# Performance work log

Measured on AMD Instinct MI355X. Metric: run time of the kernel, lower is better.

The kernel has to match this reference:

```python
import jax, jax.numpy as jnp
import numpy as np
import math

B, S, D, H, L, DFF, NHEADS_OUT = 2, 1024, 1024, 16, 4, 4096, 3
DK = D // H
LN_EPS = 1e-5


def setup_inputs() -> dict:
    key = jax.random.key(0)
    ks = jax.random.split(key, 16)
    w = lambda k, shp: jax.random.normal(k, shp, dtype=jnp.float32) * 0.02
    return {
        "src": jax.random.normal(ks[0], (B, S, 1), dtype=jnp.float32),
        "emb_w": w(ks[1], (1, D)), "emb_b": jnp.zeros((D,), jnp.float32),
        "pe": w(ks[2], (S, D)),
        "Wq": w(ks[3], (L, D, D)), "bq": jnp.zeros((L, D), jnp.float32),
        "Wk": w(ks[4], (L, D, D)), "bk": jnp.zeros((L, D), jnp.float32),
        "Wv": w(ks[5], (L, D, D)), "bv": jnp.zeros((L, D), jnp.float32),
        "Wo": w(ks[6], (L, D, D)), "bo": jnp.zeros((L, D), jnp.float32),
        "fc1_w": w(ks[7], (L, D, DFF)), "fc1_b": jnp.zeros((L, DFF), jnp.float32),
        "fc2_w": w(ks[8], (L, DFF, D)), "fc2_b": jnp.zeros((L, D), jnp.float32),
        "ln1_g": jnp.ones((L, D), jnp.float32), "ln1_b": jnp.zeros((L, D), jnp.float32),
        "ln2_g": jnp.ones((L, D), jnp.float32), "ln2_b": jnp.zeros((L, D), jnp.float32),
        "hw1": w(ks[9], (NHEADS_OUT, D, D)), "hb1": jnp.zeros((NHEADS_OUT, D), jnp.float32),
        "hw2": w(ks[10], (NHEADS_OUT, D, 1)), "hb2": jnp.zeros((NHEADS_OUT, 1), jnp.float32),
    }


def _layernorm(x, g, b):
    mu = jnp.mean(x, axis=-1, keepdims=True)
    var = jnp.mean((x - mu) ** 2, axis=-1, keepdims=True)
    return (x - mu) * jax.lax.rsqrt(var + LN_EPS) * g + b


def _custom_softmax(x):
    # faithful to module's custom_softmax: max (inf->0), exp, sum + 1e-9
    m = jnp.max(x, axis=-1, keepdims=True)
    m = jnp.where(jnp.isinf(m), 0.0, m)
    e = jnp.exp(x - m)
    return e / (jnp.sum(e, axis=-1, keepdims=True) + 1e-9)


def _attention(x, Wq, bq, Wk, bk, Wv, bv, Wo, bo, mask):
    b, s, d = x.shape
    split = lambda t: t.reshape(b, s, H, DK).transpose(0, 2, 1, 3)  # [B,H,S,DK]
    q = split(x @ Wq + bq)
    k = split(x @ Wk + bk)
    v = split(x @ Wv + bv)
    scores = jnp.einsum('bhqd,bhkd->bhqk', q, k) / math.sqrt(DK)
    scores = jnp.where(mask, scores, -jnp.inf)
    probs = _custom_softmax(scores)
    out = jnp.einsum('bhqk,bhkd->bhqd', probs, v)
    out = out.transpose(0, 2, 1, 3).reshape(b, s, d)
    return out @ Wo + bo


def reference(src, emb_w, emb_b, pe, Wq, bq, Wk, bk, Wv, bv, Wo, bo,
              fc1_w, fc1_b, fc2_w, fc2_b, ln1_g, ln1_b, ln2_g, ln2_b,
              hw1, hb1, hw2, hb2):
    s = src.shape[1]
    mask = jnp.tril(jnp.ones((s, s), dtype=bool))[None, None]  # causal [1,1,S,S]
    x = src @ emb_w + emb_b          # [B,S,D]
    x = x + pe[:s]                   # learned positional encoding
    for l in range(L):
        attn = _attention(x, Wq[l], bq[l], Wk[l], bk[l], Wv[l], bv[l], Wo[l], bo[l], mask)
        h = _layernorm(x + attn, ln1_g[l], ln1_b[l])
        x = h + attn                 # quirk in original forward_step
        ff = jax.nn.relu(jax.nn.relu(x @ fc1_w[l] + fc1_b[l]) @ fc2_w[l] + fc2_b[l])
        h2 = _layernorm(x + ff, ln2_g[l], ln2_b[l])
        x = h2 + ff                  # quirk in original forward_step
    # output_size independent 2-layer heads, each -> scalar; stack on last dim
    hid = jax.nn.relu(jnp.einsum('bsd,odf->bsof', x, hw1) + hb1[None, None])  # [B,S,3,D]
    out = jnp.einsum('bsof,ofe->bsoe', hid, hw2) + hb2[None, None]            # [B,S,3,1]
    return out[..., 0]               # [B,S,3]
```

## Files before the change

### kernel.cpp

```cpp
#include <hip/hip_runtime.h>
#include <hip/hip_bf16.h>


#define BB 2
#define SS 1024
#define DD 1024
#define HH 16
#define LL 4
#define DFFC 4096
#define DKC 64

typedef __attribute__((ext_vector_type(8))) short short8;
typedef __attribute__((ext_vector_type(4))) float f32x4;

#define GLD16(gptr, ldsptr) \
    __builtin_amdgcn_global_load_lds( \
        (const __attribute__((address_space(1))) unsigned int*)(gptr), \
        (__attribute__((address_space(3))) unsigned int*)(ldsptr), 16, 0, 0)

__device__ __forceinline__ float ldin(const void* p, long long i, int isbf) {
    if (isbf) {
        unsigned int u = ((unsigned int)((const unsigned short*)p)[i]) << 16;
        return __uint_as_float(u);
    }
    return ((const float*)p)[i];
}
__device__ __forceinline__ unsigned short f2bf(float f) {
    unsigned int u = __float_as_uint(f);
    return (unsigned short)((u + 0x7FFFu + ((u >> 16) & 1u)) >> 16);
}
__device__ __forceinline__ float bf2f(unsigned short h) {
    return __uint_as_float(((unsigned int)h) << 16);
}

__global__ void k_detect(const void* __restrict__ ln1g, int* __restrict__ flag) {
    unsigned int w = *(const unsigned int*)ln1g;
    *flag = (w == 0x3F800000u) ? 0 : 1;
}

__global__ void k_embed(const void* __restrict__ src, const void* __restrict__ emb_w,
                        const void* __restrict__ emb_b, const void* __restrict__ pe,
                        float* __restrict__ x, unsigned short* __restrict__ xb,
                        const int* __restrict__ flag) {
    int row = blockIdx.x;
    int s = row & (SS - 1);
    int isbf = *flag;
    float sv = ldin(src, row, isbf);
    for (int d = threadIdx.x; d < DD; d += 256) {
        float v = sv * ldin(emb_w, d, isbf) + ldin(emb_b, d, isbf) + ldin(pe, (long long)s * DD + d, isbf);
        x[(long long)row * DD + d] = v;
        xb[(long long)row * DD + d] = f2bf(v);
    }
}

struct TSlot { const void* src; long long off; int ldw; int nrows; int ncols; long long dstoff; };
struct TArgs { TSlot s[4]; };

__global__ __launch_bounds__(256) void k_wtrans(TArgs ta, unsigned short* __restrict__ dst,
                                                const int* __restrict__ flag) {
    TSlot sl = ta.s[blockIdx.z];
    if (!sl.src) return;
    int k0 = blockIdx.x * 64, n0 = blockIdx.y * 64;
    if (k0 >= sl.nrows || n0 >= sl.ncols) return;
    int isbf = *flag;
    __shared__ float tile[64][65];
    int tid = threadIdx.x;
    int c = tid & 63, rg = tid >> 6;
    #pragma unroll
    for (int i = 0; i < 16; i++) {
        int kr = rg * 16 + i;
        tile[kr][c] = ldin(sl.src, sl.off + (long long)(k0 + kr) * sl.ldw + n0 + c, isbf);
    }
    __syncthreads();
    int nr = tid >> 2, kc = (tid & 3) * 16;
    unsigned short* dp = dst + sl.dstoff + (long long)(n0 + nr) * sl.nrows + k0 + kc;
    unsigned short h[16];
    #pragma unroll
    for (int j = 0; j < 16; j++) h[j] = f2bf(tile[kc + j][nr]);
    uint4 u0, u1;
    u0.x = h[0] | (h[1] << 16);  u0.y = h[2] | (h[3] << 16);
    u0.z = h[4] | (h[5] << 16);  u0.w = h[6] | (h[7] << 16);
    u1.x = h[8] | (h[9] << 16);  u1.y = h[10] | (h[11] << 16);
    u1.z = h[12] | (h[13] << 16); u1.w = h[14] | (h[15] << 16);
    *(uint4*)&dp[0] = u0;
    *(uint4*)&dp[8] = u1;
}

template <int NF>
__global__ __launch_bounds__(256) void k_gemm_mfma(
    const unsigned short* __restrict__ A, int lda,
    const unsigned short* __restrict__ Wt,
    const void* b0, const void* b1, const void* b2,
    long long o0, long long o1, long long o2,
    float* __restrict__ C, int ldc,
    unsigned short* __restrict__ Cb, int ldcb,
    int K, int act, int accum, const int* __restrict__ flag)
{
    const int BN = 32 * NF;
    __shared__ __align__(16) unsigned short As[2][128 * 32];
    __shared__ __align__(16) unsigned short Bs[2][BN * 32];
    int bflag = *flag;
    int tid = threadIdx.x;
    int wave = tid >> 6, lane = tid & 63, quad = lane >> 4, l16 = lane & 15;
    int wm = (wave & 1) * 64, wn = (wave >> 1) * 16 * NF;
    int bm = blockIdx.y * 128, bn = blockIdx.x * BN;
    int srow = lane >> 2;
    int scol = (lane & 3) * 8;

    f32x4 acc[4][NF];
    #pragma unroll
    for (int i = 0; i < 4; i++)
        #pragma unroll
        for (int j = 0; j < NF; j++) acc[i][j] = (f32x4){0.f, 0.f, 0.f, 0.f};

    const unsigned short* Abase = A + (size_t)bm * lda;

    auto stage = [&](int k0, int p) {
        #pragma unroll
        for (int i = 0; i < 2; i++) {
            int s = wave * 2 + i;
            GLD16(Abase + (size_t)(s * 16 + srow) * lda + k0 + scol, &As[p][(s * 16) * 32]);
        }
        if (NF == 4) {
            #pragma unroll
            for (int i = 0; i < 2; i++) {
                int s = wave * 2 + i;
                GLD16(Wt + (size_t)(bn + s * 16 + srow) * K + k0 + scol, &Bs[p][(s * 16) * 32]);
            }
        } else {
            GLD16(Wt + (size_t)(bn + wave * 16 + srow) * K + k0 + scol, &Bs[p][(wave * 16) * 32]);
        }
    };

    int nk = K >> 5;
    stage(0, 0);
    for (int it = 0; it < nk; it++) {
        int p = it & 1;
        __syncthreads();
        if (it + 1 < nk) stage((it + 1) << 5, p ^ 1);

        short8 af[4], bf[NF];
        #pragma unroll
        for (int mi = 0; mi < 4; mi++)
            af[mi] = *(const short8*)&As[p][(wm + mi * 16 + l16) * 32 + quad * 8];
        #pragma unroll
        for (int ni = 0; ni < NF; ni++)
            bf[ni] = *(const short8*)&Bs[p][(wn + ni * 16 + l16) * 32 + quad * 8];
        #pragma unroll
        for (int mi = 0; mi < 4; mi++)
            #pragma unroll
            for (int ni = 0; ni < NF; ni++)
                acc[mi][ni] = __builtin_amdgcn_mfma_f32_16x16x32_bf16(af[mi], bf[ni], acc[mi][ni], 0, 0, 0);
    }

    #pragma unroll
    for (int ni = 0; ni < NF; ni++) {
        int cn = bn + wn + ni * 16 + l16;
        float bval = 0.0f;
        if (b0) {
            int sel = cn >> 10;
            const void* bp = (sel == 0) ? b0 : (sel == 1) ? b1 : b2;
            long long oo = (sel == 0) ? o0 : (sel == 1) ? o1 : o2;
            bval = ldin(bp, oo + (cn - (sel << 10)), bflag);
        }
        #pragma unroll
        for (int mi = 0; mi < 4; mi++) {
            #pragma unroll
            for (int rr = 0; rr < 4; rr++) {
                int cm = bm + wm + mi * 16 + quad * 4 + rr;
                float v = acc[mi][ni][rr] + bval;
                if (accum) v += C[(size_t)cm * ldc + cn];
                if (act) v = fmaxf(v, 0.0f);
                if (C) C[(size_t)cm * ldc + cn] = v;
                if (Cb) Cb[(size_t)cm * ldcb + cn] = f2bf(v);
            }
        }
    }
}

__global__ __launch_bounds__(256) void k_attn(unsigned short* __restrict__ qkv)
{
    __shared__ __align__(16) unsigned short Vt[2][64 * 72];
    __shared__ __align__(16) unsigned short Ps[4][16 * 72];

    int tid = threadIdx.x;
    int wave = tid >> 6, lane = tid & 63, quad = lane >> 4, l16 = lane & 15;
    int qt = 15 - blockIdx.x;
    int bh = blockIdx.y;
    int b = bh >> 4, h = bh & 15;
    int q0 = qt * 64;
    int qbase = q0 + wave * 16;

    const unsigned short* qrow = qkv + (size_t)(b * SS + qbase + l16) * 3072 + h * DKC;
    short8 aq0 = *(const short8*)(qrow + quad * 8);
    short8 aq1 = *(const short8*)(qrow + 32 + quad * 8);

    f32x4 oacc[4];
    #pragma unroll
    for (int nt = 0; nt < 4; nt++) oacc[nt] = (f32x4){0.f, 0.f, 0.f, 0.f};
    float rsum[4] = {0.f, 0.f, 0.f, 0.f};

    int kp = tid & 31;
    int vc = (tid >> 5) * 8;
    unsigned short* pw = &Ps[wave][0];

    auto stageV = [&](int k0, int p) {
        const unsigned short* v0 = qkv + (size_t)(b * SS + k0 + 2 * kp) * 3072 + 2048 + h * DKC + vc;
        short8 s0 = *(const short8*)v0;
        short8 s1 = *(const short8*)(v0 + 3072);
        unsigned int* vt32 = (unsigned int*)&Vt[p][0];
        #pragma unroll
        for (int i = 0; i < 8; i++) {
            unsigned int pr = ((unsigned int)(unsigned short)s0[i]) |
                              (((unsigned int)(unsigned short)s1[i]) << 16);
            vt32[(vc + i) * 36 + kp] = pr;
        }
    };

    stageV(0, 0);
    for (int kt = 0; kt <= qt; kt++) {
        int k0 = kt * 64;
        int p = kt & 1;
        __syncthreads();
        if (kt < qt) stageV(k0 + 64, p ^ 1);

        short8 bk0[4], bk1[4];
        #pragma unroll
        for (int nt = 0; nt < 4; nt++) {
            const unsigned short* krow =
                qkv + (size_t)(b * SS + k0 + nt * 16 + l16) * 3072 + 1024 + h * DKC + quad * 8;
            bk0[nt] = *(const short8*)(krow);
            bk1[nt] = *(const short8*)(krow + 32);
        }

        f32x4 sacc[4];
        #pragma unroll
        for (int nt = 0; nt < 4; nt++) {
            sacc[nt] = (f32x4){0.f, 0.f, 0.f, 0.f};
            sacc[nt] = __builtin_amdgcn_mfma_f32_16x16x32_bf16(aq0, bk0[nt], sacc[nt], 0, 0, 0);
            sacc[nt] = __builtin_amdgcn_mfma_f32_16x16x32_bf16(aq1, bk1[nt], sacc[nt], 0, 0, 0);
        }

        #pragma unroll
        for (int nt = 0; nt < 4; nt++) {
            int key = k0 + nt * 16 + l16;
            #pragma unroll
            for (int rr = 0; rr < 4; rr++) {
                float pv = __expf(sacc[nt][rr] * 0.125f);
                if (key > qbase + quad * 4 + rr) pv = 0.0f;
                rsum[rr] += pv;
                pw[(quad * 4 + rr) * 72 + nt * 16 + l16] = f2bf(pv);
            }
        }

        short8 ap0 = *(const short8*)&pw[l16 * 72 + quad * 8];
        short8 ap1 = *(const short8*)&pw[l16 * 72 + 32 + quad * 8];
        #pragma unroll
        for (int nt = 0; nt < 4; nt++) {
            short8 bv0 = *(const short8*)&Vt[p][(nt * 16 + l16) * 72 + quad * 8];
            short8 bv1 = *(const short8*)&Vt[p][(nt * 16 + l16) * 72 + 32 + quad * 8];
            oacc[nt] = __builtin_amdgcn_mfma_f32_16x16x32_bf16(ap0, bv0, oacc[nt], 0, 0, 0);
            oacc[nt] = __builtin_amdgcn_mfma_f32_16x16x32_bf16(ap1, bv1, oacc[nt], 0, 0, 0);
        }
    }

    #pragma unroll
    for (int m = 1; m < 16; m <<= 1) {
        #pragma unroll
        for (int rr = 0; rr < 4; rr++)
            rsum[rr] += __shfl_xor(rsum[rr], m, 64);
    }
    float inv[4];
    #pragma unroll
    for (int rr = 0; rr < 4; rr++) inv[rr] = 1.0f / (rsum[rr] + 1e-9f);
    #pragma unroll
    for (int rr = 0; rr < 4; rr++) {
        size_t obase = (size_t)(b * SS + qbase + quad * 4 + rr) * 3072 + h * DKC;
        #pragma unroll
        for (int nt = 0; nt < 4; nt++)
            qkv[obase + nt * 16 + l16] = f2bf(oacc[nt][rr] * inv[rr]);
    }
}

__global__ __launch_bounds__(256) void k_addlnadd(float* __restrict__ x, const float* __restrict__ t,
                                                  const void* __restrict__ g, long long goff,
                                                  const void* __restrict__ bta, long long boff,
                                                  unsigned short* __restrict__ xb,
                                                  const int* __restrict__ flag)
{
    int row = blockIdx.x;
    int tid = threadIdx.x;
    int isbf = *flag;
    __shared__ float red[256];
    long long base = (long long)row * DD;

    float yv[4], tv[4];
    float lsum = 0.0f;
    #pragma unroll
    for (int i = 0; i < 4; i++) {
        int d = tid + i * 256;
        tv[i] = t[base + d];
        yv[i] = x[base + d] + tv[i];
        lsum += yv[i];
    }
    red[tid] = lsum;
    __syncthreads();
    for (int s = 128; s > 0; s >>= 1) {
        if (tid < s) red[tid] += red[tid + s];
        __syncthreads();
    }
    float mu = red[0] * (1.0f / DD);
    __syncthreads();

    float lv = 0.0f;
    #pragma unroll
    for (int i = 0; i < 4; i++) {
        float dl = yv[i] - mu;
        lv += dl * dl;
    }
    red[tid] = lv;
    __syncthreads();
    for (int s = 128; s > 0; s >>= 1) {
        if (tid < s) red[tid] += red[tid + s];
        __syncthreads();
    }
    float rs = rsqrtf(red[0] * (1.0f / DD) + 1e-5f);

    #pragma unroll
    for (int i = 0; i < 4; i++) {
        int d = tid + i * 256;
        float nrm = (yv[i] - mu) * rs * ldin(g, goff + d, isbf) + ldin(bta, boff + d, isbf);
        float xo = nrm + tv[i];
        x[base + d] = xo;
        xb[base + d] = f2bf(xo);
    }
}

__global__ __launch_bounds__(256) void k_head(const unsigned short* __restrict__ hid,
                                              const void* __restrict__ hw2,
                                              const void* __restrict__ hb2,
                                              void* __restrict__ out,
                                              const int* __restrict__ flag)
{
    int row = blockIdx.x;
    int o = blockIdx.y;
    int tid = threadIdx.x;
    int isbf = *flag;
    __shared__ float red[256];
    long long base = (long long)row * 3072 + o * 1024;
    float acc = 0.0f;
    for (int f = tid; f < DD; f += 256)
        acc += bf2f(hid[base + f]) * ldin(hw2, (long long)o * DD + f, isbf);
    red[tid] = acc;
    __syncthreads();
    for (int s = 128; s > 0; s >>= 1) {
        if (tid < s) red[tid] += red[tid + s];
        __syncthreads();
    }
    if (tid == 0) {
        float r = red[0] + ldin(hb2, o, isbf);
        long long idx = (long long)row * 3 + o;
        if (isbf) ((__hip_bfloat16*)out)[idx] = __float2bfloat16(r);
        else      ((float*)out)[idx] = r;
    }
}

extern "C" void kernel_launch(void* const* d_in, const int* in_sizes, int n_in,
                              void* d_out, int out_size, void* d_ws, size_t ws_size,
                              hipStream_t stream) {
    char* w = (char*)d_ws;
    int* flag = (int*)w;
    const size_t NA = (size_t)BB * SS * DD;
    float* x  = (float*)(w + 256);
    float* tb = x + NA;
    unsigned short* qkv = (unsigned short*)(tb + NA);
    unsigned short* hb  = qkv + (size_t)BB * SS * 3072;
    unsigned short* wbuf = hb + (size_t)BB * SS * 2048;
    unsigned short* xb = wbuf + 4 * (size_t)DD * DD;

    const long long MM = (long long)DD * DD;
    dim3 blk(256);
    TSlot z = {nullptr, 0, 1, 0, 0, 0};

    k_detect<<<1, 1, 0, stream>>>(d_in[16], flag);
    k_embed<<<BB * SS, blk, 0, stream>>>(d_in[0], d_in[1], d_in[2], d_in[3], x, xb, flag);

    for (int l = 0; l < LL; l++) {
        long long wo = (long long)l * MM;
        long long bo = (long long)l * DD;
        {
            TArgs ta = {{ {d_in[4],  wo, DD, DD, DD, 0},
                          {d_in[6],  wo, DD, DD, DD, MM},
                          {d_in[8],  wo, DD, DD, DD, 2 * MM},
                          {d_in[10], wo, DD, DD, DD, 3 * MM} }};
            k_wtrans<<<dim3(16, 16, 4), blk, 0, stream>>>(ta, wbuf, flag);
        }
        k_gemm_mfma<4><<<dim3(24, 16), blk, 0, stream>>>(
            xb, DD, wbuf, d_in[5], d_in[7], d_in[9], bo, bo, bo,
            nullptr, 0, qkv, 3072, DD, 0, 0, flag);
        k_attn<<<dim3(16, BB * HH), blk, 0, stream>>>(qkv);
        k_gemm_mfma<2><<<dim3(16, 16), blk, 0, stream>>>(
            qkv, 3072, wbuf + 3 * MM, d_in[11], d_in[11], d_in[11], bo, bo, bo,
            tb, DD, nullptr, 0, DD, 0, 0, flag);
        k_addlnadd<<<BB * SS, blk, 0, stream>>>(x, tb, d_in[16], bo, d_in[17], bo, xb, flag);
        for (int c = 0; c < 2; c++) {
            long long w1off = (long long)l * DD * DFFC + (long long)c * 2048;
            long long b1off = (long long)l * DFFC + (long long)c * 2048;
            long long w2off = (long long)l * DFFC * DD + (long long)c * 2048 * DD;
            {
                TArgs ta = {{ {d_in[12], w1off, DFFC, DD, 2048, 0},
                              {d_in[14], w2off, DD, 2048, DD, 2 * MM}, z, z }};
                k_wtrans<<<dim3(32, 32, 2), blk, 0, stream>>>(ta, wbuf, flag);
            }
            k_gemm_mfma<4><<<dim3(16, 16), blk, 0, stream>>>(
                xb, DD, wbuf, d_in[13], d_in[13], d_in[13], b1off, b1off + 1024, 0,
                nullptr, 0, hb, 2048, DD, 1, 0, flag);
            k_gemm_mfma<2><<<dim3(16, 16), blk, 0, stream>>>(
                hb, 2048, wbuf + 2 * MM,
                (c == 1) ? d_in[15] : nullptr, d_in[15], d_in[15], bo, bo, bo,
                tb, DD, nullptr, 0, 2048, (c == 1) ? 1 : 0, c, flag);
        }
        k_addlnadd<<<BB * SS, blk, 0, stream>>>(x, tb, d_in[18], bo, d_in[19], bo, xb, flag);
    }

    {
        TArgs ta = {{ {d_in[20], 0 * MM, DD, DD, DD, 0},
                      {d_in[20], 1 * MM, DD, DD, DD, MM},
                      {d_in[20], 2 * MM, DD, DD, DD, 2 * MM}, z }};
        k_wtrans<<<dim3(16, 16, 3), blk, 0, stream>>>(ta, wbuf, flag);
    }
    k_gemm_mfma<4><<<dim3(24, 16), blk, 0, stream>>>(
        xb, DD, wbuf, d_in[21], d_in[21], d_in[21], 0, 1024, 2048,
        nullptr, 0, qkv, 3072, DD, 1, 0, flag);
    k_head<<<dim3(BB * SS, 3), blk, 0, stream>>>(qkv, d_in[22], d_in[23], d_out, flag);
}
```

Measured before the change: 1.363 ms.

## Split causal attention over key range and shrink GEMM tiles for more blocks

Attention now runs as two blocks per query tile, each covering half the causal key range. Each writes unnormalized fp32 partial outputs and row sums to scratch buffers, and a new combine kernel adds the halves, normalizes, and writes bf16 into the qkv buffer. The GEMM kernel gains an M-fragment template parameter so all GEMMs use smaller 128x64 or 64x64 tiles, which doubles the grid sizes. The aim is better occupancy of the many compute units, in exchange for an extra kernel launch, fp32 partial traffic through memory, and less operand reuse per tile.

```diff
diff --git a/kernel.cpp b/kernel.cpp
--- a/kernel.cpp
+++ b/kernel.cpp
@@ -86,7 +86,7 @@
     *(uint4*)&dp[8] = u1;
 }
 
-template <int NF>
+template <int MF, int NF>
 __global__ __launch_bounds__(256) void k_gemm_mfma(
     const unsigned short* __restrict__ A, int lda,
     const unsigned short* __restrict__ Wt,
@@ -96,20 +96,21 @@
     unsigned short* __restrict__ Cb, int ldcb,
     int K, int act, int accum, const int* __restrict__ flag)
 {
+    const int BM = 32 * MF;
     const int BN = 32 * NF;
-    __shared__ __align__(16) unsigned short As[2][128 * 32];
+    __shared__ __align__(16) unsigned short As[2][BM * 32];
     __shared__ __align__(16) unsigned short Bs[2][BN * 32];
     int bflag = *flag;
     int tid = threadIdx.x;
     int wave = tid >> 6, lane = tid & 63, quad = lane >> 4, l16 = lane & 15;
-    int wm = (wave & 1) * 64, wn = (wave >> 1) * 16 * NF;
-    int bm = blockIdx.y * 128, bn = blockIdx.x * BN;
+    int wm = (wave & 1) * 16 * MF, wn = (wave >> 1) * 16 * NF;
+    int bm = blockIdx.y * BM, bn = blockIdx.x * BN;
     int srow = lane >> 2;
     int scol = (lane & 3) * 8;
 
-    f32x4 acc[4][NF];
-    #pragma unroll
-    for (int i = 0; i < 4; i++)
+    f32x4 acc[MF][NF];
+    #pragma unroll
+    for (int i = 0; i < MF; i++)
         #pragma unroll
         for (int j = 0; j < NF; j++) acc[i][j] = (f32x4){0.f, 0.f, 0.f, 0.f};
 
@@ -117,18 +118,14 @@
 
     auto stage = [&](int k0, int p) {
         #pragma unroll
-        for (int i = 0; i < 2; i++) {
-            int s = wave * 2 + i;
+        for (int i = 0; i < MF / 2; i++) {
+            int s = wave * (MF / 2) + i;
             GLD16(Abase + (size_t)(s * 16 + srow) * lda + k0 + scol, &As[p][(s * 16) * 32]);
         }
-        if (NF == 4) {
-            #pragma unroll
-            for (int i = 0; i < 2; i++) {
-                int s = wave * 2 + i;
-                GLD16(Wt + (size_t)(bn + s * 16 + srow) * K + k0 + scol, &Bs[p][(s * 16) * 32]);
-            }
-        } else {
-            GLD16(Wt + (size_t)(bn + wave * 16 + srow) * K + k0 + scol, &Bs[p][(wave * 16) * 32]);
+        #pragma unroll
+        for (int i = 0; i < NF / 2; i++) {
+            int s = wave * (NF / 2) + i;
+            GLD16(Wt + (size_t)(bn + s * 16 + srow) * K + k0 + scol, &Bs[p][(s * 16) * 32]);
         }
     };
 
@@ -139,15 +136,15 @@
         __syncthreads();
         if (it + 1 < nk) stage((it + 1) << 5, p ^ 1);
 
-        short8 af[4], bf[NF];
-        #pragma unroll
-        for (int mi = 0; mi < 4; mi++)
+        short8 af[MF], bf[NF];
+        #pragma unroll
+        for (int mi = 0; mi < MF; mi++)
             af[mi] = *(const short8*)&As[p][(wm + mi * 16 + l16) * 32 + quad * 8];
         #pragma unroll
         for (int ni = 0; ni < NF; ni++)
             bf[ni] = *(const short8*)&Bs[p][(wn + ni * 16 + l16) * 32 + quad * 8];
         #pragma unroll
-        for (int mi = 0; mi < 4; mi++)
+        for (int mi = 0; mi < MF; mi++)
             #pragma unroll
             for (int ni = 0; ni < NF; ni++)
                 acc[mi][ni] = __builtin_amdgcn_mfma_f32_16x16x32_bf16(af[mi], bf[ni], acc[mi][ni], 0, 0, 0);
@@ -164,7 +161,7 @@
             bval = ldin(bp, oo + (cn - (sel << 10)), bflag);
         }
         #pragma unroll
-        for (int mi = 0; mi < 4; mi++) {
+        for (int mi = 0; mi < MF; mi++) {
             #pragma unroll
             for (int rr = 0; rr < 4; rr++) {
                 int cm = bm + wm + mi * 16 + quad * 4 + rr;
@@ -178,7 +175,10 @@
     }
 }
 
-__global__ __launch_bounds__(256) void k_attn(unsigned short* __restrict__ qkv)
+__global__ __launch_bounds__(256) void k_attn(const unsigned short* __restrict__ qkv,
+                                              float* __restrict__ part0,
+                                              float* __restrict__ part1,
+                                              float* __restrict__ rs)
 {
     __shared__ __align__(16) unsigned short Vt[2][64 * 72];
     __shared__ __align__(16) unsigned short Ps[4][16 * 72];
@@ -187,9 +187,15 @@
     int wave = tid >> 6, lane = tid & 63, quad = lane >> 4, l16 = lane & 15;
     int qt = 15 - blockIdx.x;
     int bh = blockIdx.y;
+    int split = blockIdx.z;
     int b = bh >> 4, h = bh & 15;
     int q0 = qt * 64;
     int qbase = q0 + wave * 16;
+
+    int nk = qt + 1;
+    int half = (nk + 1) >> 1;
+    int kt0 = split ? half : 0;
+    int kt1 = split ? nk : half;
 
     const unsigned short* qrow = qkv + (size_t)(b * SS + qbase + l16) * 3072 + h * DKC;
     short8 aq0 = *(const short8*)(qrow + quad * 8);
@@ -217,12 +223,12 @@
         }
     };
 
-    stageV(0, 0);
-    for (int kt = 0; kt <= qt; kt++) {
+    if (kt0 < kt1) stageV(kt0 * 64, 0);
+    for (int kt = kt0; kt < kt1; kt++) {
         int k0 = kt * 64;
-        int p = kt & 1;
+        int p = (kt - kt0) & 1;
         __syncthreads();
-        if (kt < qt) stageV(k0 + 64, p ^ 1);
+        if (kt + 1 < kt1) stageV(k0 + 64, p ^ 1);
 
         short8 bk0[4], bk1[4];
         #pragma unroll
@@ -270,16 +276,40 @@
         for (int rr = 0; rr < 4; rr++)
             rsum[rr] += __shfl_xor(rsum[rr], m, 64);
     }
-    float inv[4];
-    #pragma unroll
-    for (int rr = 0; rr < 4; rr++) inv[rr] = 1.0f / (rsum[rr] + 1e-9f);
+    float* part = split ? part1 : part0;
     #pragma unroll
     for (int rr = 0; rr < 4; rr++) {
-        size_t obase = (size_t)(b * SS + qbase + quad * 4 + rr) * 3072 + h * DKC;
+        int q = qbase + quad * 4 + rr;
+        size_t obase = (size_t)(b * SS + q) * 1024 + h * DKC;
         #pragma unroll
         for (int nt = 0; nt < 4; nt++)
-            qkv[obase + nt * 16 + l16] = f2bf(oacc[nt][rr] * inv[rr]);
-    }
+            part[obase + nt * 16 + l16] = oacc[nt][rr];
+        if (l16 == 0)
+            rs[(((size_t)split * 2 + b) * 16 + h) * 1024 + q] = rsum[rr];
+    }
+}
+
+__global__ __launch_bounds__(256) void k_comb(const float* __restrict__ p0,
+                                              const float* __restrict__ p1,
+                                              const float* __restrict__ rs,
+                                              unsigned short* __restrict__ qkv)
+{
+    int row = blockIdx.x;
+    int b = row >> 10, q = row & 1023;
+    int tid = threadIdx.x;
+    int col = tid * 4;
+    int h = col >> 6;
+    float r0 = rs[(((size_t)0 + b) * 16 + h) * 1024 + q];
+    float r1 = rs[(((size_t)2 + b) * 16 + h) * 1024 + q];
+    float inv = 1.0f / (r0 + r1 + 1e-9f);
+    size_t base = (size_t)row * 1024 + col;
+    float4 a = *(const float4*)(p0 + base);
+    float4 c = *(const float4*)(p1 + base);
+    unsigned short* dst = qkv + (size_t)row * 3072 + col;
+    uint2 w;
+    w.x = f2bf((a.x + c.x) * inv) | (f2bf((a.y + c.y) * inv) << 16);
+    w.y = f2bf((a.z + c.z) * inv) | (f2bf((a.w + c.w) * inv) << 16);
+    *(uint2*)dst = w;
 }
 
 __global__ __launch_bounds__(256) void k_addlnadd(float* __restrict__ x, const float* __restrict__ t,
@@ -377,6 +407,7 @@
     unsigned short* hb  = qkv + (size_t)BB * SS * 3072;
     unsigned short* wbuf = hb + (size_t)BB * SS * 2048;
     unsigned short* xb = wbuf + 4 * (size_t)DD * DD;
+    float* rsbuf = (float*)(xb + NA);
 
     const long long MM = (long long)DD * DD;
     dim3 blk(256);
@@ -395,11 +426,12 @@
                           {d_in[10], wo, DD, DD, DD, 3 * MM} }};
             k_wtrans<<<dim3(16, 16, 4), blk, 0, stream>>>(ta, wbuf, flag);
         }
-        k_gemm_mfma<4><<<dim3(24, 16), blk, 0, stream>>>(
+        k_gemm_mfma<4, 2><<<dim3(48, 16), blk, 0, stream>>>(
             xb, DD, wbuf, d_in[5], d_in[7], d_in[9], bo, bo, bo,
             nullptr, 0, qkv, 3072, DD, 0, 0, flag);
-        k_attn<<<dim3(16, BB * HH), blk, 0, stream>>>(qkv);
-        k_gemm_mfma<2><<<dim3(16, 16), blk, 0, stream>>>(
+        k_attn<<<dim3(16, BB * HH, 2), blk, 0, stream>>>(qkv, tb, (float*)hb, rsbuf);
+        k_comb<<<BB * SS, blk, 0, stream>>>(tb, (float*)hb, rsbuf, qkv);
+        k_gemm_mfma<2, 2><<<dim3(16, 32), blk, 0, stream>>>(
             qkv, 3072, wbuf + 3 * MM, d_in[11], d_in[11], d_in[11], bo, bo, bo,
             tb, DD, nullptr, 0, DD, 0, 0, flag);
         k_addlnadd<<<BB * SS, blk, 0, stream>>>(x, tb, d_in[16], bo, d_in[17], bo, xb, flag);
@@ -412,10 +444,10 @@
                               {d_in[14], w2off, DD, 2048, DD, 2 * MM}, z, z }};
                 k_wtrans<<<dim3(32, 32, 2), blk, 0, stream>>>(ta, wbuf, flag);
             }
-            k_gemm_mfma<4><<<dim3(16, 16), blk, 0, stream>>>(
+            k_gemm_mfma<4, 2><<<dim3(32, 16), blk, 0, stream>>>(
                 xb, DD, wbuf, d_in[13], d_in[13], d_in[13], b1off, b1off + 1024, 0,
                 nullptr, 0, hb, 2048, DD, 1, 0, flag);
-            k_gemm_mfma<2><<<dim3(16, 16), blk, 0, stream>>>(
+            k_gemm_mfma<2, 2><<<dim3(16, 32), blk, 0, stream>>>(
                 hb, 2048, wbuf + 2 * MM,
                 (c == 1) ? d_in[15] : nullptr, d_in[15], d_in[15], bo, bo, bo,
                 tb, DD, nullptr, 0, 2048, (c == 1) ? 1 : 0, c, flag);
@@ -429,7 +461,7 @@
                       {d_in[20], 2 * MM, DD, DD, DD, 2 * MM}, z }};
         k_wtrans<<<dim3(16, 16, 3), blk, 0, stream>>>(ta, wbuf, flag);
     }
-    k_gemm_mfma<4><<<dim3(24, 16), blk, 0, stream>>>(
+    k_gemm_mfma<4, 2><<<dim3(48, 16), blk, 0, stream>>>(
         xb, DD, wbuf, d_in[21], d_in[21], d_in[21], 0, 1024, 2048,
         nullptr, 0, qkv, 3072, DD, 1, 0, flag);
     k_head<<<dim3(BB * SS, 3), blk, 0, stream>>>(qkv, d_in[22], d_in[23], d_out, flag);
```

Measured after the change: 1.231 ms. 9.7% less time.
